# Optimization experiments

Hardware: AMD Instinct MI355X
Metric: run time of the kernel (lower is better)

## Reference

```python
import jax, jax.numpy as jnp
import numpy as np

DIM = 4096
N_HEADS = 32
N_KV_HEADS = 8
HEAD_DIM = DIM // N_HEADS  # 128
KV_DIM = N_KV_HEADS * HEAD_DIM  # 1024
B, T = 2, 1024


def setup_inputs() -> dict:
    key = jax.random.key(0)
    ks = jax.random.split(key, 5)
    s1 = 1.0 / np.sqrt(DIM)
    return {
        "x": jax.random.normal(ks[0], (B, T, DIM), dtype=jnp.float32),
        "W1": jax.random.uniform(ks[1], (DIM + 2 * KV_DIM, DIM), dtype=jnp.float32, minval=-s1, maxval=s1),
        "b1": jax.random.uniform(ks[2], (DIM + 2 * KV_DIM,), dtype=jnp.float32, minval=-s1, maxval=s1),
        "W2": jax.random.uniform(ks[3], (DIM, DIM), dtype=jnp.float32, minval=-s1, maxval=s1),
        "b2": jax.random.uniform(ks[4], (DIM,), dtype=jnp.float32, minval=-s1, maxval=s1),
    }


def reference(x, W1, b1, W2, b2):
    Bn, Tn, D = x.shape
    G = N_HEADS // N_KV_HEADS
    qkv = x @ W1.T + b1  # [B,T,D+2*KV_DIM]
    q = qkv[:, :, :DIM]
    k = qkv[:, :, DIM:DIM + KV_DIM]
    v = qkv[:, :, DIM + KV_DIM:]
    # Faithful to torch repeat_interleave(G, dim=-1): scalar-level interleave on flat feature dim
    k = jnp.repeat(k, G, axis=-1)  # [B,T,D]
    v = jnp.repeat(v, G, axis=-1)
    q = q.reshape(Bn, Tn, N_HEADS, HEAD_DIM).transpose(0, 2, 1, 3)  # [B,H,T,hd]
    k = k.reshape(Bn, Tn, N_HEADS, HEAD_DIM).transpose(0, 2, 1, 3)
    v = v.reshape(Bn, Tn, N_HEADS, HEAD_DIM).transpose(0, 2, 1, 3)
    scale = 1.0 / jnp.sqrt(jnp.asarray(HEAD_DIM, dtype=x.dtype))
    qk = jnp.einsum('bhqd,bhkd->bhqk', q, k) * scale  # [B,H,T,T]
    causal = jnp.tril(jnp.ones((Tn, Tn), dtype=bool))
    qk = jnp.where(causal[None, None], qk, jnp.asarray(-jnp.inf, dtype=qk.dtype))
    att = jax.nn.softmax(qk, axis=-1)
    out = jnp.einsum('bhqk,bhkd->bhqd', att, v)  # [B,H,T,hd]
    out = out.transpose(0, 2, 1, 3).reshape(Bn, Tn, D)
    return out @ W2.T + b2
```

## Files before the change

kernel.cpp:

```cpp
#include <hip/hip_runtime.h>

#define DIMX  4096
#define NH    32
#define HD    128
#define BB    2
#define TT    1024
#define MROWS (BB*TT)
#define CQKV  3072
#define SCALE_Q 0.12751743f

typedef _Float16 half_t;
typedef __attribute__((ext_vector_type(4))) _Float16 f16x4;
typedef __attribute__((ext_vector_type(8))) _Float16 f16x8;
typedef __attribute__((ext_vector_type(4))) float    f32x4;

__device__ __forceinline__ void async_copy16(const void* gsrc, void* ldst) {
  __builtin_amdgcn_global_load_lds(
      (const __attribute__((address_space(1))) unsigned int*)gsrc,
      (__attribute__((address_space(3))) unsigned int*)ldst,
      16, 0, 0);
}

__global__ __launch_bounds__(256) void cvt_f32_f16_kernel(
    const float4* __restrict__ src, f16x4* __restrict__ dst, int n4) {
  int stride = gridDim.x * blockDim.x;
  for (int i = blockIdx.x * blockDim.x + threadIdx.x; i < n4; i += stride) {
    float4 f = src[i];
    f16x4 h;
    h.x = (_Float16)f.x; h.y = (_Float16)f.y;
    h.z = (_Float16)f.z; h.w = (_Float16)f.w;
    dst[i] = h;
  }
}

__global__ __launch_bounds__(256) void fold_w1_kernel(
    const float* __restrict__ W1, const float* __restrict__ b1,
    half_t* __restrict__ W1f, float* __restrict__ b1f)
{
  long idx = (long)blockIdx.x * 256 + threadIdx.x;
  int row = (int)(idx >> 10);
  int c4  = ((int)idx & 1023) << 2;
  f16x4 h;
  if (row < 1024) {
    const float* s = W1 + ((long)row << 2) * DIMX + c4;
    float4 a = *(const float4*)s;
    float4 b = *(const float4*)(s + DIMX);
    float4 c = *(const float4*)(s + 2 * DIMX);
    float4 d = *(const float4*)(s + 3 * DIMX);
    h.x = (_Float16)((a.x + b.x + c.x + d.x) * SCALE_Q);
    h.y = (_Float16)((a.y + b.y + c.y + d.y) * SCALE_Q);
    h.z = (_Float16)((a.z + b.z + c.z + d.z) * SCALE_Q);
    h.w = (_Float16)((a.w + b.w + c.w + d.w) * SCALE_Q);
    if (c4 == 0) {
      const float* bb = b1 + ((long)row << 2);
      b1f[row] = (bb[0] + bb[1] + bb[2] + bb[3]) * SCALE_Q;
    }
  } else {
    const float* s = W1 + ((long)(row + 3072)) * DIMX + c4;
    float4 a = *(const float4*)s;
    h.x = (_Float16)a.x; h.y = (_Float16)a.y;
    h.z = (_Float16)a.z; h.w = (_Float16)a.w;
    if (c4 == 0) b1f[row] = b1[row + 3072];
  }
  *(f16x4*)&W1f[(long)row * DIMX + c4] = h;
}

__global__ __launch_bounds__(256) void fold_w2_kernel(
    const float* __restrict__ W2, half_t* __restrict__ W2f)
{
  long idx = (long)blockIdx.x * 256 + threadIdx.x;
  int row = (int)(idx >> 8);
  int j4  = ((int)idx & 255) << 2;
  const float* s = W2 + (long)row * DIMX + ((long)j4 << 2);
  float4 a = *(const float4*)s;
  float4 b = *(const float4*)(s + 4);
  float4 c = *(const float4*)(s + 8);
  float4 d = *(const float4*)(s + 12);
  f16x4 h;
  h.x = (_Float16)(a.x + a.y + a.z + a.w);
  h.y = (_Float16)(b.x + b.y + b.z + b.w);
  h.z = (_Float16)(c.x + c.y + c.z + c.w);
  h.w = (_Float16)(d.x + d.y + d.z + d.w);
  *(f16x4*)&W2f[(long)row * 1024 + j4] = h;
}


__global__ __launch_bounds__(256, 3) void gemm_nt_splitk(
    const half_t* __restrict__ A, const half_t* __restrict__ Bw,
    float* __restrict__ Cp0, float* __restrict__ Cp1,
    int M, int N, int K)
{
  __shared__ alignas(16) half_t As[128 * 64];
  __shared__ alignas(16) half_t Bs[128 * 64];

  const int tid  = threadIdx.x;
  const int lane = tid & 63;
  const int w    = tid >> 6;
  const long row0 = (long)blockIdx.y * 128;
  const long col0 = (long)blockIdx.x * 128;
  const int  KH   = K >> 1;
  const long k0   = (long)blockIdx.z * KH;

  const int rr = tid >> 3;
  const int cs = (((tid & 7) ^ (rr & 7)) << 3);
  const half_t* ga[4]; const half_t* gb[4];
#pragma unroll
  for (int i = 0; i < 4; ++i) {
    ga[i] = A  + (row0 + i * 32 + rr) * K + k0 + cs;
    gb[i] = Bw + (col0 + i * 32 + rr) * K + k0 + cs;
  }
  half_t* lds_a = &As[w * 512];
  half_t* lds_b = &Bs[w * 512];

  const int wm = (w >> 1) * 64;
  const int wn = (w & 1) * 64;
  const int fr   = lane & 15;
  const int quad = lane >> 4;
  const int rsw  = fr & 7;
  const int o0 = ((quad ^ rsw) << 3);
  const int o1 = (((quad | 4) ^ rsw) << 3);
  const half_t* paw = &As[(wm + fr) * 64];
  const half_t* pbw = &Bs[(wn + fr) * 64];

  f32x4 acc[4][4] = {};

  for (int kt = 0; kt < KH; kt += 64) {
    __syncthreads();
#pragma unroll
    for (int i = 0; i < 4; ++i) async_copy16(ga[i] + kt, lds_a + i * 2048);
#pragma unroll
    for (int i = 0; i < 4; ++i) async_copy16(gb[i] + kt, lds_b + i * 2048);
    __syncthreads();

    f16x8 af[4], bf[4];
#pragma unroll
    for (int mi = 0; mi < 4; ++mi) af[mi] = *(const f16x8*)(paw + mi * 1024 + o0);
#pragma unroll
    for (int ni = 0; ni < 4; ++ni) bf[ni] = *(const f16x8*)(pbw + ni * 1024 + o0);
#pragma unroll
    for (int mi = 0; mi < 4; ++mi)
#pragma unroll
      for (int ni = 0; ni < 4; ++ni)
        acc[mi][ni] = __builtin_amdgcn_mfma_f32_16x16x32_f16(
            af[mi], bf[ni], acc[mi][ni], 0, 0, 0);

#pragma unroll
    for (int mi = 0; mi < 4; ++mi) af[mi] = *(const f16x8*)(paw + mi * 1024 + o1);
#pragma unroll
    for (int ni = 0; ni < 4; ++ni) bf[ni] = *(const f16x8*)(pbw + ni * 1024 + o1);
#pragma unroll
    for (int mi = 0; mi < 4; ++mi)
#pragma unroll
      for (int ni = 0; ni < 4; ++ni)
        acc[mi][ni] = __builtin_amdgcn_mfma_f32_16x16x32_f16(
            af[mi], bf[ni], acc[mi][ni], 0, 0, 0);
  }

  float* Cp = blockIdx.z ? Cp1 : Cp0;
  const int er = (lane >> 4) * 4;
  const int ec = lane & 15;
#pragma unroll
  for (int mi = 0; mi < 4; ++mi) {
#pragma unroll
    for (int ni = 0; ni < 4; ++ni) {
      long gn = col0 + wn + ni * 16 + ec;
#pragma unroll
      for (int r = 0; r < 4; ++r) {
        long gm = row0 + wm + mi * 16 + er + r;
        Cp[gm * N + gn] = acc[mi][ni][r];
      }
    }
  }
}

template<int OUT_IS_F16>
__global__ __launch_bounds__(256, 3) void gemm_nt_bias(
    const half_t* __restrict__ A, const half_t* __restrict__ Bw,
    const float* __restrict__ bias, void* __restrict__ Cout,
    int M, int N, int K)
{
  __shared__ alignas(16) half_t As[128 * 64];
  __shared__ alignas(16) half_t Bs[128 * 64];

  const int tid  = threadIdx.x;
  const int lane = tid & 63;
  const int w    = tid >> 6;
  const long row0 = (long)blockIdx.y * 128;
  const long col0 = (long)blockIdx.x * 128;

  const int rr = tid >> 3;
  const int cs = (((tid & 7) ^ (rr & 7)) << 3);
  const half_t* ga[4]; const half_t* gb[4];
#pragma unroll
  for (int i = 0; i < 4; ++i) {
    ga[i] = A  + (row0 + i * 32 + rr) * K + cs;
    gb[i] = Bw + (col0 + i * 32 + rr) * K + cs;
  }
  half_t* lds_a = &As[w * 512];
  half_t* lds_b = &Bs[w * 512];

  const int wm = (w >> 1) * 64;
  const int wn = (w & 1) * 64;
  const int fr   = lane & 15;
  const int quad = lane >> 4;
  const int rsw  = fr & 7;
  const int o0 = ((quad ^ rsw) << 3);
  const int o1 = (((quad | 4) ^ rsw) << 3);
  const half_t* paw = &As[(wm + fr) * 64];
  const half_t* pbw = &Bs[(wn + fr) * 64];

  f32x4 acc[4][4] = {};

  for (int kt = 0; kt < K; kt += 64) {
    __syncthreads();
#pragma unroll
    for (int i = 0; i < 4; ++i) async_copy16(ga[i] + kt, lds_a + i * 2048);
#pragma unroll
    for (int i = 0; i < 4; ++i) async_copy16(gb[i] + kt, lds_b + i * 2048);
    __syncthreads();

    f16x8 af[4], bf[4];
#pragma unroll
    for (int mi = 0; mi < 4; ++mi) af[mi] = *(const f16x8*)(paw + mi * 1024 + o0);
#pragma unroll
    for (int ni = 0; ni < 4; ++ni) bf[ni] = *(const f16x8*)(pbw + ni * 1024 + o0);
#pragma unroll
    for (int mi = 0; mi < 4; ++mi)
#pragma unroll
      for (int ni = 0; ni < 4; ++ni)
        acc[mi][ni] = __builtin_amdgcn_mfma_f32_16x16x32_f16(
            af[mi], bf[ni], acc[mi][ni], 0, 0, 0);

#pragma unroll
    for (int mi = 0; mi < 4; ++mi) af[mi] = *(const f16x8*)(paw + mi * 1024 + o1);
#pragma unroll
    for (int ni = 0; ni < 4; ++ni) bf[ni] = *(const f16x8*)(pbw + ni * 1024 + o1);
#pragma unroll
    for (int mi = 0; mi < 4; ++mi)
#pragma unroll
      for (int ni = 0; ni < 4; ++ni)
        acc[mi][ni] = __builtin_amdgcn_mfma_f32_16x16x32_f16(
            af[mi], bf[ni], acc[mi][ni], 0, 0, 0);
  }

  const int er = (lane >> 4) * 4;
  const int ec = lane & 15;
#pragma unroll
  for (int mi = 0; mi < 4; ++mi) {
#pragma unroll
    for (int ni = 0; ni < 4; ++ni) {
      long gn = col0 + wn + ni * 16 + ec;
      float bv = bias[gn];
#pragma unroll
      for (int r = 0; r < 4; ++r) {
        long gm = row0 + wm + mi * 16 + er + r;
        float v = acc[mi][ni][r] + bv;
        if (OUT_IS_F16) ((half_t*)Cout)[gm * N + gn] = (half_t)v;
        else            ((float*)Cout)[gm * N + gn]  = v;
      }
    }
  }
}

__global__ __launch_bounds__(256) void splitk_reduce_kernel(
    const float4* __restrict__ C0, const float4* __restrict__ C1,
    const float4* __restrict__ bias4, f16x4* __restrict__ dst)
{
  const int col  = blockIdx.x * 256 + threadIdx.x;
  const long row = blockIdx.y;
  const long i   = row * (CQKV / 4) + col;
  float4 a = C0[i];
  float4 b = C1[i];
  float4 bv = bias4[col];
  f16x4 h;
  h.x = (_Float16)(a.x + b.x + bv.x);
  h.y = (_Float16)(a.y + b.y + bv.y);
  h.z = (_Float16)(a.z + b.z + bv.z);
  h.w = (_Float16)(a.w + b.w + bv.w);
  dst[i] = h;
}

__global__ __launch_bounds__(256) void v_transpose_kernel(
    const half_t* __restrict__ qkvc, half_t* __restrict__ vt)
{
  __shared__ half_t lt[64][72];
  const int t  = threadIdx.x;
  const int b  = blockIdx.z;
  const int d0 = blockIdx.x * 64;
  const int k0 = blockIdx.y * 64;
  const int tl = t >> 3;
  const int dc = (t & 7) * 8;

  const half_t* src = qkvc + ((long)b * TT + k0 + tl) * CQKV + 2048 + d0 + dc;
  *(f16x8*)&lt[tl][dc]      = *(const f16x8*)src;
  *(f16x8*)&lt[tl + 32][dc] = *(const f16x8*)(src + 32 * CQKV);
  __syncthreads();

  half_t* dstp = vt + ((long)b * 1024 + d0 + tl) * 1024 + k0 + dc;
  f16x8 o0, o1;
#pragma unroll
  for (int j = 0; j < 8; ++j) {
    o0[j] = lt[dc + j][tl];
    o1[j] = lt[dc + j][tl + 32];
  }
  *(f16x8*)dstp = o0;
  *(f16x8*)(dstp + 32 * 1024) = o1;
}

#define PSS 72
__global__ __launch_bounds__(256, 4) void attn_kernel(
    const half_t* __restrict__ qkv,
    const half_t* __restrict__ vt,
    half_t* __restrict__ attc)
{
  __shared__ alignas(16) half_t Ks[32 * 64];
  __shared__ alignas(16) half_t Vs[32 * 64];
  __shared__ alignas(16) half_t Ps[4][16 * PSS];

  const int tid  = threadIdx.x;
  const int lane = tid & 63;
  const int w    = tid >> 6;
  const int low  = lane & 15;
  const int quad = lane >> 4;
  const int bh   = blockIdx.y;
  const int b    = bh >> 5;
  const int h    = bh & 31;
  const long rb  = (long)b * TT;

  const int su  = tid >> 3;
  const int sp  = tid & 7;
  const int spx = sp ^ (su & 7);
  const half_t* kg = qkv + (rb + 2 * su + (spx >> 2)) * CQKV + 1024
                         + h * 32 + (spx & 3) * 8;
  const half_t* vg = vt + ((long)b * 1024 + h * 32 + su) * 1024 + spx * 8;
  half_t* kdst = &Ks[w * 512];
  half_t* vdst = &Vs[w * 512];
  half_t* psw  = &Ps[w][0];
  float*  Ob   = (float*)psw;

  const int tile = blockIdx.x;
  const int t0   = tile * 64;
  const int qg   = t0 + 16 * w;

  f16x8 qf = *(const f16x8*)&qkv[(rb + qg + low) * CQKV + h * 32 + quad * 8];

  f16x8 onesf;
#pragma unroll
  for (int i = 0; i < 8; ++i) onesf[i] = (_Float16)1.0f;

  f32x4 acc0 = {}, acc1 = {}, acc2 = {};
  const f32x4 zero = {};

  const int dsw = low & 7;
  const int ksw = (low >> 1) & 7;
  const int kp  = (((low & 1) << 2) | quad) ^ ksw;

  for (int c = 0; c <= t0; c += 64) {
    __syncthreads();
    async_copy16(kg + (long)c * CQKV, kdst);
    async_copy16(vg + c, vdst);
    __syncthreads();

    f32x4 s[4];
#pragma unroll
    for (int st = 0; st < 4; ++st) {
      const int u = st * 8 + (low >> 1);
      f16x8 kf = *(const f16x8*)&Ks[u * 64 + kp * 8];
      s[st] = __builtin_amdgcn_mfma_f32_16x16x32_f16(qf, kf, zero, 0, 0, 0);
    }

    const bool diag = (c == t0);
#pragma unroll
    for (int st = 0; st < 4; ++st) {
#pragma unroll
      for (int r = 0; r < 4; ++r) {
        const int key = c + st * 16 + low;
        const int q   = qg + 4 * quad + r;
        float p = __builtin_amdgcn_exp2f(s[st][r]);
        if (diag && key > q) p = 0.f;
        psw[(4 * quad + r) * PSS + st * 16 + low] = (_Float16)p;
      }
    }

    f16x8 p0 = *(const f16x8*)&psw[low * PSS + 0 * 32 + quad * 8];
    f16x8 p1 = *(const f16x8*)&psw[low * PSS + 1 * 32 + quad * 8];

    f16x8 v00 = *(const f16x8*)&Vs[(0  + low) * 64 + ((0 + quad) ^ dsw) * 8];
    f16x8 v01 = *(const f16x8*)&Vs[(0  + low) * 64 + ((4 + quad) ^ dsw) * 8];
    f16x8 v10 = *(const f16x8*)&Vs[(16 + low) * 64 + ((0 + quad) ^ dsw) * 8];
    f16x8 v11 = *(const f16x8*)&Vs[(16 + low) * 64 + ((4 + quad) ^ dsw) * 8];

    acc0 = __builtin_amdgcn_mfma_f32_16x16x32_f16(v00,   p0, acc0, 0, 0, 0);
    acc0 = __builtin_amdgcn_mfma_f32_16x16x32_f16(v01,   p1, acc0, 0, 0, 0);
    acc1 = __builtin_amdgcn_mfma_f32_16x16x32_f16(v10,   p0, acc1, 0, 0, 0);
    acc1 = __builtin_amdgcn_mfma_f32_16x16x32_f16(v11,   p1, acc1, 0, 0, 0);
    acc2 = __builtin_amdgcn_mfma_f32_16x16x32_f16(onesf, p0, acc2, 0, 0, 0);
    acc2 = __builtin_amdgcn_mfma_f32_16x16x32_f16(onesf, p1, acc2, 0, 0, 0);
  }

  __syncthreads();

  float linv = 1.0f / acc2[0];

#pragma unroll
  for (int r = 0; r < 4; ++r) {
    Ob[low * 36 + 0  + 4 * quad + r] = acc0[r] * linv;
    Ob[low * 36 + 16 + 4 * quad + r] = acc1[r] * linv;
  }
  __syncthreads();

  f16x8 ov;
#pragma unroll
  for (int i = 0; i < 8; ++i)
    ov[i] = (_Float16)Ob[low * 36 + quad * 8 + i];
  *(f16x8*)&attc[(rb + qg + low) * 1024 + h * 32 + quad * 8] = ov;
}

extern "C" void kernel_launch(void* const* d_in, const int* in_sizes, int n_in,
                              void* d_out, int out_size, void* d_ws, size_t ws_size,
                              hipStream_t stream) {
  (void)in_sizes; (void)n_in; (void)out_size; (void)ws_size;
  const float* x  = (const float*)d_in[0];
  const float* W1 = (const float*)d_in[1];
  const float* b1 = (const float*)d_in[2];
  const float* W2 = (const float*)d_in[3];
  const float* b2 = (const float*)d_in[4];
  float* out = (float*)d_out;

  const size_t nX   = (size_t)MROWS * DIMX;
  const size_t nW1f = (size_t)CQKV  * DIMX;
  const size_t nW2f = (size_t)DIMX  * 1024;
  const size_t nQKV = (size_t)MROWS * CQKV;
  const size_t nATT = (size_t)MROWS * 1024;

  half_t* ws   = (half_t*)d_ws;
  half_t* xh   = ws;
  half_t* w1f  = xh   + nX;
  half_t* w2f  = w1f  + nW1f;
  half_t* qkvc = w2f  + nW2f;
  half_t* attc = qkvc + nQKV;
  float*  b1f  = (float*)(attc + nATT);
  float*  c1   = (float*)(b1f + 4096);
  half_t* vt   = xh;

  cvt_f32_f16_kernel<<<4096, 256, 0, stream>>>((const float4*)x, (f16x4*)xh,
                                               (int)(nX / 4));
  fold_w1_kernel<<<12288, 256, 0, stream>>>(W1, b1, w1f, b1f);
  fold_w2_kernel<<<4096, 256, 0, stream>>>(W2, w2f);

  gemm_nt_splitk<<<dim3(CQKV / 128, MROWS / 128, 2), 256, 0, stream>>>(
      xh, w1f, out , c1 , MROWS, CQKV, DIMX);
  splitk_reduce_kernel<<<dim3(CQKV / 4 / 256, MROWS), 256, 0, stream>>>(
      (const float4*)out, (const float4*)c1, (const float4*)b1f,
      (f16x4*)qkvc);

  v_transpose_kernel<<<dim3(16, 16, BB), 256, 0, stream>>>(qkvc, vt);

  attn_kernel<<<dim3(16, BB * NH), 256, 0, stream>>>(qkvc, vt, attc);

  gemm_nt_bias<0><<<dim3(DIMX / 128, MROWS / 128), 256, 0, stream>>>(
      attc, w2f, b2, (void*)out, MROWS, DIMX, 1024);
}
```

Measured before the change: 352.1 us.

## Fuse V split-K reduce into transpose and swizzle block order for XCD locality

The split-K reduction now covers only the Q/K columns, and the V part is reduced, bias-added and converted to fp16 directly inside the transpose kernel. This removes one fp16 write and re-read of V. Both GEMMs and the attention kernel remap their flat block index so that blocks dispatched round-robin across the eight XCDs land on contiguous tiles, which should improve L2 reuse. The attention kernel also drops its occupancy hint of 4 from launch_bounds, which may change register allocation.

```diff
diff --git a/kernel.cpp b/kernel.cpp
--- a/kernel.cpp
+++ b/kernel.cpp
@@ -96,10 +96,19 @@
   const int tid  = threadIdx.x;
   const int lane = tid & 63;
   const int w    = tid >> 6;
-  const long row0 = (long)blockIdx.y * 128;
-  const long col0 = (long)blockIdx.x * 128;
+
+  const int GX = gridDim.x, GY = gridDim.y;
+  const int total = GX * GY * gridDim.z;
+  const int flat  = blockIdx.x + GX * (blockIdx.y + GY * blockIdx.z);
+  const int swz   = (flat & 7) * (total >> 3) + (flat >> 3);
+  const int bx = swz % GX;
+  const int by = (swz / GX) % GY;
+  const int bz = swz / (GX * GY);
+
+  const long row0 = (long)by * 128;
+  const long col0 = (long)bx * 128;
   const int  KH   = K >> 1;
-  const long k0   = (long)blockIdx.z * KH;
+  const long k0   = (long)bz * KH;
 
   const int rr = tid >> 3;
   const int cs = (((tid & 7) ^ (rr & 7)) << 3);
@@ -156,7 +165,7 @@
             af[mi], bf[ni], acc[mi][ni], 0, 0, 0);
   }
 
-  float* Cp = blockIdx.z ? Cp1 : Cp0;
+  float* Cp = bz ? Cp1 : Cp0;
   const int er = (lane >> 4) * 4;
   const int ec = lane & 15;
 #pragma unroll
@@ -185,8 +194,17 @@
   const int tid  = threadIdx.x;
   const int lane = tid & 63;
   const int w    = tid >> 6;
-  const long row0 = (long)blockIdx.y * 128;
-  const long col0 = (long)blockIdx.x * 128;
+
+  const int GX = gridDim.x, GY = gridDim.y;
+  const int GXq = GX >> 2, GYh = GY >> 1;
+  const int flat = blockIdx.x + GX * blockIdx.y;
+  const int k8   = flat & 7;
+  const int i8   = flat >> 3;
+  const int bx = (k8 & 3) * GXq + (i8 % GXq);
+  const int by = (k8 >> 2) * GYh + (i8 / GXq);
+
+  const long row0 = (long)by * 128;
+  const long col0 = (long)bx * 128;
 
   const int rr = tid >> 3;
   const int cs = (((tid & 7) ^ (rr & 7)) << 3);
@@ -280,8 +298,9 @@
   dst[i] = h;
 }
 
-__global__ __launch_bounds__(256) void v_transpose_kernel(
-    const half_t* __restrict__ qkvc, half_t* __restrict__ vt)
+__global__ __launch_bounds__(256) void v_reduce_transpose_kernel(
+    const float* __restrict__ C0, const float* __restrict__ C1,
+    const float* __restrict__ bias, half_t* __restrict__ vt)
 {
   __shared__ half_t lt[64][72];
   const int t  = threadIdx.x;
@@ -291,9 +310,27 @@
   const int tl = t >> 3;
   const int dc = (t & 7) * 8;
 
-  const half_t* src = qkvc + ((long)b * TT + k0 + tl) * CQKV + 2048 + d0 + dc;
-  *(f16x8*)&lt[tl][dc]      = *(const f16x8*)src;
-  *(f16x8*)&lt[tl + 32][dc] = *(const f16x8*)(src + 32 * CQKV);
+  const long base0 = ((long)b * TT + k0 + tl) * CQKV + 2048 + d0 + dc;
+  float4 bv0 = *(const float4*)(bias + 2048 + d0 + dc);
+  float4 bv1 = *(const float4*)(bias + 2048 + d0 + dc + 4);
+#pragma unroll
+  for (int half = 0; half < 2; ++half) {
+    const long base = base0 + (long)half * 32 * CQKV;
+    float4 a0 = *(const float4*)(C0 + base);
+    float4 a1 = *(const float4*)(C0 + base + 4);
+    float4 c0 = *(const float4*)(C1 + base);
+    float4 c1 = *(const float4*)(C1 + base + 4);
+    f16x8 hvec;
+    hvec[0] = (_Float16)(a0.x + c0.x + bv0.x);
+    hvec[1] = (_Float16)(a0.y + c0.y + bv0.y);
+    hvec[2] = (_Float16)(a0.z + c0.z + bv0.z);
+    hvec[3] = (_Float16)(a0.w + c0.w + bv0.w);
+    hvec[4] = (_Float16)(a1.x + c1.x + bv1.x);
+    hvec[5] = (_Float16)(a1.y + c1.y + bv1.y);
+    hvec[6] = (_Float16)(a1.z + c1.z + bv1.z);
+    hvec[7] = (_Float16)(a1.w + c1.w + bv1.w);
+    *(f16x8*)&lt[tl + half * 32][dc] = hvec;
+  }
   __syncthreads();
 
   half_t* dstp = vt + ((long)b * 1024 + d0 + tl) * 1024 + k0 + dc;
@@ -308,7 +345,7 @@
 }
 
 #define PSS 72
-__global__ __launch_bounds__(256, 4) void attn_kernel(
+__global__ __launch_bounds__(256) void attn_kernel(
     const half_t* __restrict__ qkv,
     const half_t* __restrict__ vt,
     half_t* __restrict__ attc)
@@ -322,7 +359,11 @@
   const int w    = tid >> 6;
   const int low  = lane & 15;
   const int quad = lane >> 4;
-  const int bh   = blockIdx.y;
+
+  const int flat = blockIdx.x + 16 * blockIdx.y;
+  const int swz  = (flat & 7) * 128 + (flat >> 3);
+  const int tile = swz & 15;
+  const int bh   = swz >> 4;
   const int b    = bh >> 5;
   const int h    = bh & 31;
   const long rb  = (long)b * TT;
@@ -338,7 +379,6 @@
   half_t* psw  = &Ps[w][0];
   float*  Ob   = (float*)psw;
 
-  const int tile = blockIdx.x;
   const int t0   = tile * 64;
   const int qg   = t0 + 16 * w;
 
@@ -450,11 +490,12 @@
 
   gemm_nt_splitk<<<dim3(CQKV / 128, MROWS / 128, 2), 256, 0, stream>>>(
       xh, w1f, out , c1 , MROWS, CQKV, DIMX);
-  splitk_reduce_kernel<<<dim3(CQKV / 4 / 256, MROWS), 256, 0, stream>>>(
+
+  splitk_reduce_kernel<<<dim3(2, MROWS), 256, 0, stream>>>(
       (const float4*)out, (const float4*)c1, (const float4*)b1f,
       (f16x4*)qkvc);
-
-  v_transpose_kernel<<<dim3(16, 16, BB), 256, 0, stream>>>(qkvc, vt);
+  v_reduce_transpose_kernel<<<dim3(16, 16, BB), 256, 0, stream>>>(
+      out, c1, b1f, vt);
 
   attn_kernel<<<dim3(16, BB * NH), 256, 0, stream>>>(qkvc, vt, attc);
 
```

Result: no change. 350.2 us (-0.5%).
